# Kernel optimization log

Measured on AMD Instinct MI355X. Metric: run time of the kernel, lower is better.

The kernel has to match this reference:

```python
import jax, jax.numpy as jnp
import numpy as np

D = 50          # half-window
K = 2 * D + 1   # 101 window positions
P_SIZE = 100    # predictive-alignment hidden dim


def setup_inputs() -> dict:
    key = jax.random.key(0)
    ks = jax.random.split(key, 5)
    B, S, CQ, CC = 2, 2048, 256, 256
    q = jax.random.normal(ks[0], (B, S, CQ), jnp.float32)
    c_t = jax.random.normal(ks[1], (B, S, CC), jnp.float32)
    W_a = jax.random.normal(ks[2], (CC, CQ), jnp.float32) / np.sqrt(CQ).astype(np.float32)
    W_p = jax.random.normal(ks[3], (P_SIZE, CC), jnp.float32) / np.sqrt(CC).astype(np.float32)
    V_p = jax.random.normal(ks[4], (1, P_SIZE), jnp.float32) / np.sqrt(P_SIZE).astype(np.float32)
    return {"q": q, "c_t": c_t, "W_a": W_a, "W_p": W_p, "V_p": V_p}


def reference(q, c_t, W_a, W_p, V_p):
    B, S, CQ = q.shape
    # predictive alignment: p in (0, S), one predicted center per (b, s)
    p = S * jax.nn.sigmoid(jnp.tanh(c_t @ W_p.T) @ V_p.T)[..., 0]          # [B,S]
    offs = jnp.arange(-D, D + 1)                                           # [K]
    # torch .long() truncates toward zero (raw can be negative)
    raw = jnp.trunc(p[..., None] + offs[None, None, :] + 1.0).astype(jnp.int32)
    # clamp to [0, S+1] then mod (S+1): index 0 == padded (invalid) row,
    # matching torch's NaN-padded row 0 (S+1 wraps to 0 via the modulo)
    idx = jnp.clip(raw, 0, S + 1) % (S + 1)                                # [B,S,K]
    mask = idx == 0                                                        # invalid window slots
    # pad row 0 (torch pads with NaN then zeroes the NaN rows; we pad with 0
    # and mask by index -> identical math for finite q)
    q_pad = jnp.concatenate([jnp.zeros((B, 1, CQ), q.dtype), q], axis=1)   # [B,S+1,CQ]
    gathered = jnp.take_along_axis(q_pad, idx.reshape(B, S * K, 1), axis=1)
    q1 = jnp.where(mask[..., None], 0.0, gathered.reshape(B, S, K, CQ))    # [B,S,K,CQ]
    # score: W_a projection then dot with context
    Wq = jnp.einsum("bskq,cq->bskc", q1, W_a)                              # [B,S,K,CC]
    a = jnp.einsum("bskc,bsc->bsk", Wq, c_t)                               # [B,S,K]
    a = jnp.where(mask, -jnp.inf, a)
    attn = jax.nn.softmax(a, axis=2)                                       # [B,S,K]
    # gaussian decay centered at floor(p) (p > 0 so trunc == floor)
    exponent = -2.0 * (((offs[None, None, :] + jnp.trunc(p)[..., None] - p[..., None]) / D) ** 2)
    w = attn * jnp.exp(exponent)                                           # [B,S,K]
    s_t = jnp.einsum("bsk,bskc->bsc", w, q1)                               # [B,S,CQ]
    return s_t
```

## Files before the change

### kernel.cpp

```cpp
#include <hip/hip_runtime.h>
#include <math.h>

#define S_LEN 2048
#define NB    2
#define CQ_   256
#define CC_   256
#define DH    50
#define KW    101
#define PS    100
#define RB    8
#define HPAD  128
#define WTH   1e-5f

__global__ __launch_bounds__(128) void k_prep(const float* __restrict__ Wp,
                                              float* __restrict__ WpT) {
  const int c = blockIdx.x, j = threadIdx.x;
  WpT[c * HPAD + j] = (j < PS) ? Wp[j * CC_ + c] : 0.0f;
}

__global__ __launch_bounds__(384, 3) void k_align(const float* __restrict__ ct,
    const float* __restrict__ Wa, const float* __restrict__ WpT,
    const float* __restrict__ Vp, float* __restrict__ p_out,
    float* __restrict__ V_out) {
  const int r0  = blockIdx.x * RB;
  const int tid = threadIdx.x;
  const float* crow = ct + (size_t)r0 * CC_;

  __shared__ float red[RB][PS + 4];

  if (tid < CQ_) {
    const float* wa = Wa + tid;
    float acc[RB];
#pragma unroll
    for (int r = 0; r < RB; ++r) acc[r] = 0.0f;

    float4 cv0[RB], cv1[RB];
#pragma unroll
    for (int r = 0; r < RB; ++r) cv0[r] = *(const float4*)&crow[r * CC_];
    float w00 = wa[0 * CQ_], w01 = wa[1 * CQ_], w02 = wa[2 * CQ_], w03 = wa[3 * CQ_];

    for (int c = 0; c < CC_ - 4; c += 4) {
      const int cn = c + 4;
#pragma unroll
      for (int r = 0; r < RB; ++r) cv1[r] = *(const float4*)&crow[r * CC_ + cn];
      const float w10 = wa[(size_t)(cn + 0) * CQ_];
      const float w11 = wa[(size_t)(cn + 1) * CQ_];
      const float w12 = wa[(size_t)(cn + 2) * CQ_];
      const float w13 = wa[(size_t)(cn + 3) * CQ_];
#pragma unroll
      for (int r = 0; r < RB; ++r) {
        float t = acc[r];
        t = fmaf(cv0[r].x, w00, t);
        t = fmaf(cv0[r].y, w01, t);
        t = fmaf(cv0[r].z, w02, t);
        t = fmaf(cv0[r].w, w03, t);
        acc[r] = t;
      }
#pragma unroll
      for (int r = 0; r < RB; ++r) cv0[r] = cv1[r];
      w00 = w10; w01 = w11; w02 = w12; w03 = w13;
    }
#pragma unroll
    for (int r = 0; r < RB; ++r) {
      float t = acc[r];
      t = fmaf(cv0[r].x, w00, t);
      t = fmaf(cv0[r].y, w01, t);
      t = fmaf(cv0[r].z, w02, t);
      t = fmaf(cv0[r].w, w03, t);
      acc[r] = t;
    }
#pragma unroll
    for (int r = 0; r < RB; ++r)
      V_out[(size_t)(r0 + r) * CQ_ + tid] = acc[r];
  } else {
    const int j = tid - CQ_;
    const float* wh = WpT + j;
    float ah[RB];
#pragma unroll
    for (int r = 0; r < RB; ++r) ah[r] = 0.0f;

    float4 cv0[RB], cv1[RB];
#pragma unroll
    for (int r = 0; r < RB; ++r) cv0[r] = *(const float4*)&crow[r * CC_];
    float w00 = wh[0 * HPAD], w01 = wh[1 * HPAD], w02 = wh[2 * HPAD], w03 = wh[3 * HPAD];

    for (int c = 0; c < CC_ - 4; c += 4) {
      const int cn = c + 4;
#pragma unroll
      for (int r = 0; r < RB; ++r) cv1[r] = *(const float4*)&crow[r * CC_ + cn];
      const float w10 = wh[(size_t)(cn + 0) * HPAD];
      const float w11 = wh[(size_t)(cn + 1) * HPAD];
      const float w12 = wh[(size_t)(cn + 2) * HPAD];
      const float w13 = wh[(size_t)(cn + 3) * HPAD];
#pragma unroll
      for (int r = 0; r < RB; ++r) {
        float t = ah[r];
        t = fmaf(cv0[r].x, w00, t);
        t = fmaf(cv0[r].y, w01, t);
        t = fmaf(cv0[r].z, w02, t);
        t = fmaf(cv0[r].w, w03, t);
        ah[r] = t;
      }
#pragma unroll
      for (int r = 0; r < RB; ++r) cv0[r] = cv1[r];
      w00 = w10; w01 = w11; w02 = w12; w03 = w13;
    }
#pragma unroll
    for (int r = 0; r < RB; ++r) {
      float t = ah[r];
      t = fmaf(cv0[r].x, w00, t);
      t = fmaf(cv0[r].y, w01, t);
      t = fmaf(cv0[r].z, w02, t);
      t = fmaf(cv0[r].w, w03, t);
      ah[r] = t;
    }
    if (j < PS) {
      const float vp = Vp[j];
#pragma unroll
      for (int r = 0; r < RB; ++r) red[r][j] = vp * tanhf(ah[r]);
    }
  }
  __syncthreads();
  if (tid < RB) {
    float s = 0.0f;
    for (int j = 0; j < PS; ++j) s += red[tid][j];
    p_out[r0 + tid] = (float)S_LEN * (1.0f / (1.0f + expf(-s)));
  }
}

__global__ __launch_bounds__(256, 4) void k_attn(const float* __restrict__ q,
    const float* __restrict__ p_in, const float* V,
    float* out) {
  const int wid  = threadIdx.x >> 6;
  const int row  = (blockIdx.x << 2) + wid;
  const int lane = threadIdx.x & 63;
  const int b    = row >> 11;

  __shared__ float ss[4][128];
  __shared__ float sw[4][128];

  const float p  = p_in[row];
  const float tp = truncf(p);
  const float* qb = q + (size_t)b * S_LEN * CQ_;

  const int sub = lane >> 4;
  const int sl  = lane & 15;
  const int c4  = sl * 4;

  const float* vrow = V + (size_t)row * CQ_;
  const float4 v0 = *(const float4*)(vrow + c4);
  const float4 v1 = *(const float4*)(vrow + 64 + c4);
  const float4 v2 = *(const float4*)(vrow + 128 + c4);
  const float4 v3 = *(const float4*)(vrow + 192 + c4);

  if (lane >= KW - 64) ss[wid][64 + lane] = -INFINITY;

  for (int g = 0; g < 26; g += 2) {
    const int ka = (g << 2) + sub;
    const int kb = ka + 4;
    const float ta = p + (float)(ka - DH) + 1.0f;
    const float tb = p + (float)(kb - DH) + 1.0f;
    const int rawa = (int)ta;
    const int rawb = (int)tb;
    const bool oka = (rawa >= 1) && (rawa <= S_LEN) && (ka < KW);
    const bool okb = (rawb >= 1) && (rawb <= S_LEN) && (kb < KW);
    const float* qra = qb + (size_t)(oka ? rawa - 1 : 0) * CQ_;
    const float* qrb = qb + (size_t)(okb ? rawb - 1 : 0) * CQ_;

    const float4 a0 = *(const float4*)(qra + c4);
    const float4 a1 = *(const float4*)(qra + 64 + c4);
    const float4 a2 = *(const float4*)(qra + 128 + c4);
    const float4 a3 = *(const float4*)(qra + 192 + c4);
    const float4 b0 = *(const float4*)(qrb + c4);
    const float4 b1 = *(const float4*)(qrb + 64 + c4);
    const float4 b2 = *(const float4*)(qrb + 128 + c4);
    const float4 b3 = *(const float4*)(qrb + 192 + c4);

    float t0 = a0.x * v0.x, t1 = a1.x * v1.x, t2 = a2.x * v2.x, t3 = a3.x * v3.x;
    t0 = fmaf(a0.y, v0.y, t0); t1 = fmaf(a1.y, v1.y, t1);
    t2 = fmaf(a2.y, v2.y, t2); t3 = fmaf(a3.y, v3.y, t3);
    t0 = fmaf(a0.z, v0.z, t0); t1 = fmaf(a1.z, v1.z, t1);
    t2 = fmaf(a2.z, v2.z, t2); t3 = fmaf(a3.z, v3.z, t3);
    t0 = fmaf(a0.w, v0.w, t0); t1 = fmaf(a1.w, v1.w, t1);
    t2 = fmaf(a2.w, v2.w, t2); t3 = fmaf(a3.w, v3.w, t3);
    float sA = (t0 + t1) + (t2 + t3);
    sA += __shfl_xor(sA, 1, 64);
    sA += __shfl_xor(sA, 2, 64);
    sA += __shfl_xor(sA, 4, 64);
    sA += __shfl_xor(sA, 8, 64);
    sA = oka ? sA : -INFINITY;
    if (sl == 0) ss[wid][ka] = sA;

    float u0 = b0.x * v0.x, u1 = b1.x * v1.x, u2 = b2.x * v2.x, u3 = b3.x * v3.x;
    u0 = fmaf(b0.y, v0.y, u0); u1 = fmaf(b1.y, v1.y, u1);
    u2 = fmaf(b2.y, v2.y, u2); u3 = fmaf(b3.y, v3.y, u3);
    u0 = fmaf(b0.z, v0.z, u0); u1 = fmaf(b1.z, v1.z, u1);
    u2 = fmaf(b2.z, v2.z, u2); u3 = fmaf(b3.z, v3.z, u3);
    u0 = fmaf(b0.w, v0.w, u0); u1 = fmaf(b1.w, v1.w, u1);
    u2 = fmaf(b2.w, v2.w, u2); u3 = fmaf(b3.w, v3.w, u3);
    float sB = (u0 + u1) + (u2 + u3);
    sB += __shfl_xor(sB, 1, 64);
    sB += __shfl_xor(sB, 2, 64);
    sB += __shfl_xor(sB, 4, 64);
    sB += __shfl_xor(sB, 8, 64);
    sB = okb ? sB : -INFINITY;
    if (sl == 0) ss[wid][kb] = sB;
  }

  const float s0 = ss[wid][lane];
  const float s1 = ss[wid][64 + lane];

  float m = fmaxf(s0, s1);
#pragma unroll
  for (int off = 1; off < 64; off <<= 1) m = fmaxf(m, __shfl_xor(m, off, 64));

  const float e0 = __expf(s0 - m);
  const float e1 = __expf(s1 - m);
  float den = e0 + e1;
#pragma unroll
  for (int off = 1; off < 64; off <<= 1) den += __shfl_xor(den, off, 64);
  const float inv = 1.0f / den;

  float g0 = ((float)(lane - DH) + tp - p) / (float)DH;
  float g1 = ((float)(lane + (64 - DH)) + tp - p) / (float)DH;
  const float w0 = e0 * __expf(-2.0f * g0 * g0) * inv;
  const float w1 = e1 * __expf(-2.0f * g1 * g1) * inv;
  sw[wid][lane] = w0;
  if (lane < KW - 64) sw[wid][64 + lane] = w1;

  unsigned long long m0 = __ballot(w0 > WTH);
  unsigned long long m1 = __ballot((lane < KW - 64) && (w1 > WTH));

  float4 acc = make_float4(0.0f, 0.0f, 0.0f, 0.0f);
  while ((m0 | m1) != 0ull) {
    int kk[4];
#pragma unroll
    for (int i = 0; i < 4; ++i) {
      int k = -1;
      if (m0)      { k = __builtin_ctzll(m0);      m0 &= m0 - 1; }
      else if (m1) { k = 64 + __builtin_ctzll(m1); m1 &= m1 - 1; }
      kk[i] = k;
    }
#pragma unroll
    for (int i = 0; i < 4; ++i) {
      if (kk[i] >= 0) {
        const float wk = sw[wid][kk[i]];
        const float t = p + (float)(kk[i] - DH) + 1.0f;
        const int r = (int)t - 1;
        const float4 qv = *(const float4*)(qb + (size_t)r * CQ_ + lane * 4);
        acc.x = fmaf(wk, qv.x, acc.x);
        acc.y = fmaf(wk, qv.y, acc.y);
        acc.z = fmaf(wk, qv.z, acc.z);
        acc.w = fmaf(wk, qv.w, acc.w);
      }
    }
  }
  *(float4*)(out + (size_t)row * CQ_ + lane * 4) = acc;
}

extern "C" void kernel_launch(void* const* d_in, const int* in_sizes, int n_in,
                              void* d_out, int out_size, void* d_ws, size_t ws_size,
                              hipStream_t stream) {
  const float* q  = (const float*)d_in[0];
  const float* ct = (const float*)d_in[1];
  const float* Wa = (const float*)d_in[2];
  const float* Wp = (const float*)d_in[3];
  const float* Vp = (const float*)d_in[4];
  float* out = (float*)d_out;

  float* ws     = (float*)d_ws;
  float* p_ws   = ws;
  float* WpT_ws = ws + NB * S_LEN;

  k_prep <<<CC_, HPAD, 0, stream>>>(Wp, WpT_ws);
  k_align<<<(NB * S_LEN) / RB, 384, 0, stream>>>(ct, Wa, WpT_ws, Vp, p_ws, out);
  k_attn <<<(NB * S_LEN) / 4, 256, 0, stream>>>(q, p_ws, out, out);
}
```

Baseline: 113.1 us.

## Split each attention row across two wavefronts with shared-memory reduction

k_attn now assigns two wavefronts to each output row instead of one. Each wavefront computes half of the window scores, and the weighted-sum rows are split between them in alternating order. Partial sums are combined through shared memory and two block-wide barriers. This doubles the number of wavefronts per row to expose more parallelism and memory-level concurrency, at the cost of extra synchronisation, extra LDS traffic and a redundant softmax computed in both halves. One risk: the V row is read from the same buffer as out, and the final write now happens after the barrier, so it only covers the block's own rows.

```diff
diff --git a/kernel.cpp b/kernel.cpp
--- a/kernel.cpp
+++ b/kernel.cpp
@@ -128,16 +128,20 @@
   }
 }
 
-__global__ __launch_bounds__(256, 4) void k_attn(const float* __restrict__ q,
+__global__ __launch_bounds__(256, 8) void k_attn(const float* __restrict__ q,
     const float* __restrict__ p_in, const float* V,
     float* out) {
-  const int wid  = threadIdx.x >> 6;
-  const int row  = (blockIdx.x << 2) + wid;
-  const int lane = threadIdx.x & 63;
+  const int tid  = threadIdx.x;
+  const int wid  = tid >> 6;
+  const int rloc = wid >> 1;
+  const int half = wid & 1;
+  const int row  = (blockIdx.x << 1) + rloc;
+  const int lane = tid & 63;
   const int b    = row >> 11;
 
-  __shared__ float ss[4][128];
-  __shared__ float sw[4][128];
+  __shared__ float ss[2][128];
+  __shared__ float sw[2][128];
+  __shared__ float sacc[4][CQ_];
 
   const float p  = p_in[row];
   const float tp = truncf(p);
@@ -153,10 +157,11 @@
   const float4 v2 = *(const float4*)(vrow + 128 + c4);
   const float4 v3 = *(const float4*)(vrow + 192 + c4);
 
-  if (lane >= KW - 64) ss[wid][64 + lane] = -INFINITY;
-
-  for (int g = 0; g < 26; g += 2) {
-    const int ka = (g << 2) + sub;
+  if (lane >= KW - 64) ss[rloc][64 + lane] = -INFINITY;
+
+  for (int gg = 0; gg < 13; gg += 2) {
+    const int ga = half * 13 + gg;
+    const int ka = (ga << 2) + sub;
     const int kb = ka + 4;
     const float ta = p + (float)(ka - DH) + 1.0f;
     const float tb = p + (float)(kb - DH) + 1.0f;
@@ -189,7 +194,7 @@
     sA += __shfl_xor(sA, 4, 64);
     sA += __shfl_xor(sA, 8, 64);
     sA = oka ? sA : -INFINITY;
-    if (sl == 0) ss[wid][ka] = sA;
+    if (sl == 0 && ka < 128) ss[rloc][ka] = sA;
 
     float u0 = b0.x * v0.x, u1 = b1.x * v1.x, u2 = b2.x * v2.x, u3 = b3.x * v3.x;
     u0 = fmaf(b0.y, v0.y, u0); u1 = fmaf(b1.y, v1.y, u1);
@@ -204,11 +209,12 @@
     sB += __shfl_xor(sB, 4, 64);
     sB += __shfl_xor(sB, 8, 64);
     sB = okb ? sB : -INFINITY;
-    if (sl == 0) ss[wid][kb] = sB;
-  }
-
-  const float s0 = ss[wid][lane];
-  const float s1 = ss[wid][64 + lane];
+    if (sl == 0 && kb < 128) ss[rloc][kb] = sB;
+  }
+  __syncthreads();
+
+  const float s0 = ss[rloc][lane];
+  const float s1 = ss[rloc][64 + lane];
 
   float m = fmaxf(s0, s1);
 #pragma unroll
@@ -225,13 +231,14 @@
   float g1 = ((float)(lane + (64 - DH)) + tp - p) / (float)DH;
   const float w0 = e0 * __expf(-2.0f * g0 * g0) * inv;
   const float w1 = e1 * __expf(-2.0f * g1 * g1) * inv;
-  sw[wid][lane] = w0;
-  if (lane < KW - 64) sw[wid][64 + lane] = w1;
+  sw[rloc][lane] = w0;
+  if (lane < KW - 64) sw[rloc][64 + lane] = w1;
 
   unsigned long long m0 = __ballot(w0 > WTH);
   unsigned long long m1 = __ballot((lane < KW - 64) && (w1 > WTH));
 
   float4 acc = make_float4(0.0f, 0.0f, 0.0f, 0.0f);
+  int cnt = 0;
   while ((m0 | m1) != 0ull) {
     int kk[4];
 #pragma unroll
@@ -244,18 +251,26 @@
 #pragma unroll
     for (int i = 0; i < 4; ++i) {
       if (kk[i] >= 0) {
-        const float wk = sw[wid][kk[i]];
-        const float t = p + (float)(kk[i] - DH) + 1.0f;
-        const int r = (int)t - 1;
-        const float4 qv = *(const float4*)(qb + (size_t)r * CQ_ + lane * 4);
-        acc.x = fmaf(wk, qv.x, acc.x);
-        acc.y = fmaf(wk, qv.y, acc.y);
-        acc.z = fmaf(wk, qv.z, acc.z);
-        acc.w = fmaf(wk, qv.w, acc.w);
+        if ((cnt & 1) == half) {
+          const float wk = sw[rloc][kk[i]];
+          const float t = p + (float)(kk[i] - DH) + 1.0f;
+          const int r = (int)t - 1;
+          const float4 qv = *(const float4*)(qb + (size_t)r * CQ_ + lane * 4);
+          acc.x = fmaf(wk, qv.x, acc.x);
+          acc.y = fmaf(wk, qv.y, acc.y);
+          acc.z = fmaf(wk, qv.z, acc.z);
+          acc.w = fmaf(wk, qv.w, acc.w);
+        }
+        ++cnt;
       }
     }
   }
-  *(float4*)(out + (size_t)row * CQ_ + lane * 4) = acc;
+  *(float4*)&sacc[wid][lane * 4] = acc;
+  __syncthreads();
+
+  const int row0 = (blockIdx.x << 1);
+  out[(size_t)row0 * CQ_ + tid]       = sacc[0][tid] + sacc[1][tid];
+  out[(size_t)(row0 + 1) * CQ_ + tid] = sacc[2][tid] + sacc[3][tid];
 }
 
 extern "C" void kernel_launch(void* const* d_in, const int* in_sizes, int n_in,
@@ -274,5 +289,5 @@
 
   k_prep <<<CC_, HPAD, 0, stream>>>(Wp, WpT_ws);
   k_align<<<(NB * S_LEN) / RB, 384, 0, stream>>>(ct, Wa, WpT_ws, Vp, p_ws, out);
-  k_attn <<<(NB * S_LEN) / 4, 256, 0, stream>>>(q, p_ws, out, out);
-}
+  k_attn <<<(NB * S_LEN) / 2, 256, 0, stream>>>(q, p_ws, out, out);
+}
```

After: 111.3 us. No clear change (-1.6%).
